# Optimization experiments

Measured on AMD Instinct MI355X. Metric: run time of the kernel, lower is better.

Reference implementation:

```python
import jax, jax.numpy as jnp
import numpy as np

N = 2048

def setup_inputs() -> dict:
    key = jax.random.key(0)
    k0, k1, k2, k3 = jax.random.split(key, 4)
    return {
        "input": jax.random.normal(k0, (N, N), dtype=jnp.float32),
        "weight1": jax.random.normal(k1, (N, N), dtype=jnp.float32),
        "weight2": jax.random.normal(k2, (N, N), dtype=jnp.float32),
        "weight3": jax.random.normal(k3, (N, N), dtype=jnp.float32),
    }

def reference(input, weight1, weight2, weight3):
    # Faithful translation of the torch DAG (duplicate mm kept: t4 == t2,
    # so t8 is mathematically zero, but we preserve the original math).
    t1 = input @ weight1
    t2 = input @ weight2
    t3 = weight3 @ weight3
    t4 = input @ weight2
    t5 = t1 * weight1
    t6 = (t5 @ input) * weight1
    t7 = t1 * t2 + t1 + t3
    t8 = t2 - t4
    t9 = t7 * t8 + t6 * t3
    t11 = t3 * t9
    t12 = t3 * (t1 @ input) * t6
    t13 = t7 + t11
    t14 = t8 + t12
    t15 = t13 + t14
    return t15
```

## Files before the change

### kernel.cpp

```cpp
#include <hip/hip_runtime.h>
#include <hip/hip_bf16.h>
#include <stdint.h>

#define NN 2048

typedef __bf16 bf16;
typedef __bf16 bf16x8 __attribute__((ext_vector_type(8)));
typedef __bf16 bf16x4 __attribute__((ext_vector_type(4)));
typedef float f32x4 __attribute__((ext_vector_type(4)));

__device__ __forceinline__ void async_copy16(bf16* lds, const bf16* g) {
    __builtin_amdgcn_global_load_lds(
        (const __attribute__((address_space(1))) unsigned int*)g,
        (__attribute__((address_space(3))) unsigned int*)lds,
        16, 0, 0);
}

__global__ void transpose_cast_kernel(const float* __restrict__ in,
                                      bf16* __restrict__ outT,
                                      bf16* __restrict__ outN) {
    __shared__ float tile[32][33];
    const int bx = blockIdx.x * 32, by = blockIdx.y * 32;
    const int tx = threadIdx.x, ty = threadIdx.y;
#pragma unroll
    for (int i = 0; i < 32; i += 8) {
        float v = in[(size_t)(by + ty + i) * NN + bx + tx];
        tile[ty + i][tx] = v;
        if (outN) outN[(size_t)(by + ty + i) * NN + bx + tx] = (bf16)v;
    }
    __syncthreads();
#pragma unroll
    for (int i = 0; i < 32; i += 8)
        outT[(size_t)(bx + ty + i) * NN + by + tx] = (bf16)tile[tx][ty + i];
}

struct GemmArgs {
    const bf16* A[3];
    const bf16* Bt[3];
    float*      C[3];
};

__global__ __launch_bounds__(256) void gemm_bt_batched(GemmArgs args) {
    const bf16* __restrict__ A  = args.A[blockIdx.z];
    const bf16* __restrict__ Bt = args.Bt[blockIdx.z];
    float* __restrict__ C       = args.C[blockIdx.z];

    __shared__ bf16 As[128 * 32];
    __shared__ bf16 Bs[128 * 32];

    const int t    = threadIdx.x;
    const int bm   = blockIdx.x * 128;
    const int bn   = blockIdx.y * 128;

    const int off0 = t * 8;
    const int row0 = off0 >> 5;
    const int col0 = off0 & 31;

    const bf16* gA0 = A  + (size_t)(bm + row0) * NN + col0;
    const bf16* gB0 = Bt + (size_t)(bn + row0) * NN + col0;

    const int wave = t >> 6;
    const int lane = t & 63;
    const int wm   = (wave >> 1) * 64;
    const int wn   = (wave & 1) * 64;
    const int lrow = lane & 15;
    const int q    = lane >> 4;

    f32x4 acc[4][4];
#pragma unroll
    for (int i = 0; i < 4; ++i)
#pragma unroll
        for (int j = 0; j < 4; ++j) acc[i][j] = (f32x4){0.f, 0.f, 0.f, 0.f};

    for (int k0 = 0; k0 < NN; k0 += 32) {
        async_copy16(&As[off0],            gA0 + k0);
        async_copy16(&As[off0 + 64 * 32],  gA0 + (size_t)64 * NN + k0);
        async_copy16(&Bs[off0],            gB0 + k0);
        async_copy16(&Bs[off0 + 64 * 32],  gB0 + (size_t)64 * NN + k0);
        __syncthreads();

        bf16x8 af[4], bfr[4];
#pragma unroll
        for (int i = 0; i < 4; ++i)
            af[i] = *(const bf16x8*)&As[(wm + i * 16 + lrow) * 32 + q * 8];
#pragma unroll
        for (int j = 0; j < 4; ++j)
            bfr[j] = *(const bf16x8*)&Bs[(wn + j * 16 + lrow) * 32 + q * 8];

#pragma unroll
        for (int i = 0; i < 4; ++i)
#pragma unroll
            for (int j = 0; j < 4; ++j)
                acc[i][j] = __builtin_amdgcn_mfma_f32_16x16x32_bf16(
                    af[i], bfr[j], acc[i][j], 0, 0, 0);
        __syncthreads();
    }

#pragma unroll
    for (int i = 0; i < 4; ++i)
#pragma unroll
        for (int j = 0; j < 4; ++j)
#pragma unroll
            for (int r = 0; r < 4; ++r)
                C[(size_t)(bm + wm + i * 16 + q * 4 + r) * NN +
                  (bn + wn + j * 16 + lrow)] = acc[i][j][r];
}

__global__ void post_m1_kernel(const float* __restrict__ M1,
                               const float* __restrict__ W1,
                               bf16* __restrict__ M1bf,
                               bf16* __restrict__ B1bf) {
    const size_t i = ((size_t)blockIdx.x * 256 + threadIdx.x) * 4;
    const float4 m = *(const float4*)&M1[i];
    const float4 w = *(const float4*)&W1[i];
    bf16x4 mb = {(bf16)m.x, (bf16)m.y, (bf16)m.z, (bf16)m.w};
    bf16x4 bb = {(bf16)(m.x * w.x), (bf16)(m.y * w.y),
                 (bf16)(m.z * w.z), (bf16)(m.w * w.w)};
    *(bf16x4*)&M1bf[i] = mb;
    *(bf16x4*)&B1bf[i] = bb;
}

__global__ void epilogue_kernel(const float* __restrict__ M1,
                                const float* __restrict__ M3,
                                const float* __restrict__ M4,
                                const float* __restrict__ M5,
                                const float* __restrict__ W1,
                                float* __restrict__ out) {
    const size_t i = ((size_t)blockIdx.x * 256 + threadIdx.x) * 4;
    const float4 m1 = *(const float4*)&M1[i];
    const float4 m3 = *(const float4*)&M3[i];
    const float4 m4 = *(const float4*)&M4[i];
    const float4 m5 = *(const float4*)&M5[i];
    const float4 w1 = *(const float4*)&W1[i];
    const float4 m2 = *(const float4*)&out[i];
    float4 r;
    r.x = m1.x * m2.x + m1.x + m3.x + m3.x * (m4.x * w1.x) * (m3.x + m5.x);
    r.y = m1.y * m2.y + m1.y + m3.y + m3.y * (m4.y * w1.y) * (m3.y + m5.y);
    r.z = m1.z * m2.z + m1.z + m3.z + m3.z * (m4.z * w1.z) * (m3.z + m5.z);
    r.w = m1.w * m2.w + m1.w + m3.w + m3.w * (m4.w * w1.w) * (m3.w + m5.w);
    *(float4*)&out[i] = r;
}

extern "C" void kernel_launch(void* const* d_in, const int* in_sizes, int n_in,
                              void* d_out, int out_size, void* d_ws, size_t ws_size,
                              hipStream_t stream) {
    const float* A  = (const float*)d_in[0];
    const float* W1 = (const float*)d_in[1];
    const float* W2 = (const float*)d_in[2];
    const float* W3 = (const float*)d_in[3];
    float* out = (float*)d_out;

    const size_t P = (size_t)NN * NN;
    char* ws = (char*)d_ws;

    bf16* Abf  = (bf16*)ws;
    bf16* At   = Abf + P;
    bf16* W1t  = At + P;
    bf16* W2t  = W1t + P;
    bf16* W3bf = W2t + P;
    bf16* W3t  = W3bf + P;
    float* M1  = (float*)(W3t + P);
    float* M3  = M1 + P;
    float* M4  = M3 + P;
    float* M5  = M4 + P;

    const dim3 tb(32, 8), tg(NN / 32, NN / 32);
    transpose_cast_kernel<<<tg, tb, 0, stream>>>(A,  At,  Abf);
    transpose_cast_kernel<<<tg, tb, 0, stream>>>(W1, W1t, nullptr);
    transpose_cast_kernel<<<tg, tb, 0, stream>>>(W2, W2t, nullptr);
    transpose_cast_kernel<<<tg, tb, 0, stream>>>(W3, W3t, W3bf);

    GemmArgs g3;
    g3.A[0] = Abf;  g3.Bt[0] = W1t; g3.C[0] = M1;
    g3.A[1] = Abf;  g3.Bt[1] = W2t; g3.C[1] = out;
    g3.A[2] = W3bf; g3.Bt[2] = W3t; g3.C[2] = M3;
    gemm_bt_batched<<<dim3(NN / 128, NN / 128, 3), 256, 0, stream>>>(g3);

    bf16* M1bf = W2t;
    bf16* B1bf = W3bf;
    post_m1_kernel<<<(P / 4) / 256, 256, 0, stream>>>(M1, W1, M1bf, B1bf);

    GemmArgs g2;
    g2.A[0] = M1bf; g2.Bt[0] = At; g2.C[0] = M5;
    g2.A[1] = B1bf; g2.Bt[1] = At; g2.C[1] = M4;
    g2.A[2] = M1bf; g2.Bt[2] = At; g2.C[2] = M5;
    gemm_bt_batched<<<dim3(NN / 128, NN / 128, 2), 256, 0, stream>>>(g2);

    epilogue_kernel<<<(P / 4) / 256, 256, 0, stream>>>(M1, M3, M4, M5, W1, out);
}
```

Measured before the change: 290.1 us.

## Use 128x64 GEMM tiles with XOR-swizzled LDS and batch transpose-cast launches

Shrinks the GEMM block tile from 128x128 to 128x64, which doubles the grid size so more CUs stay busy and each thread holds fewer accumulator registers. Adds an XOR swizzle on the LDS column index, applied to both the async global-to-LDS stores and the fragment reads, to reduce bank conflicts. Merges the four transpose-cast launches into one launch using a z-dimension. In exchange, A tiles are reloaded twice as often per output element, so per-FLOP global and LDS traffic goes up.

```diff
diff --git a/kernel.cpp b/kernel.cpp
--- a/kernel.cpp
+++ b/kernel.cpp
@@ -3,6 +3,9 @@
 #include <stdint.h>
 
 #define NN 2048
+#define BM 128
+#define BN 64
+#define BK 32
 
 typedef __bf16 bf16;
 typedef __bf16 bf16x8 __attribute__((ext_vector_type(8)));
@@ -16,9 +19,16 @@
         16, 0, 0);
 }
 
-__global__ void transpose_cast_kernel(const float* __restrict__ in,
-                                      bf16* __restrict__ outT,
-                                      bf16* __restrict__ outN) {
+struct CastArgs {
+    const float* in[4];
+    bf16*        outT[4];
+    bf16*        outN[4];
+};
+
+__global__ void transpose_cast_kernel(CastArgs args) {
+    const float* __restrict__ in = args.in[blockIdx.z];
+    bf16* __restrict__ outT      = args.outT[blockIdx.z];
+    bf16* __restrict__ outN      = args.outN[blockIdx.z];
     __shared__ float tile[32][33];
     const int bx = blockIdx.x * 32, by = blockIdx.y * 32;
     const int tx = threadIdx.x, ty = threadIdx.y;
@@ -45,16 +55,17 @@
     const bf16* __restrict__ Bt = args.Bt[blockIdx.z];
     float* __restrict__ C       = args.C[blockIdx.z];
 
-    __shared__ bf16 As[128 * 32];
-    __shared__ bf16 Bs[128 * 32];
-
-    const int t    = threadIdx.x;
-    const int bm   = blockIdx.x * 128;
-    const int bn   = blockIdx.y * 128;
-
+    __shared__ bf16 As[BM * BK];
+    __shared__ bf16 Bs[BN * BK];
+
+    const int t  = threadIdx.x;
+    const int bm = blockIdx.x * BM;
+    const int bn = blockIdx.y * BN;
+
+    const int row0 = t >> 2;
+    const int qp   = t & 3;
+    const int col0 = ((qp ^ ((row0 >> 1) & 3)) << 3);
     const int off0 = t * 8;
-    const int row0 = off0 >> 5;
-    const int col0 = off0 & 31;
 
     const bf16* gA0 = A  + (size_t)(bm + row0) * NN + col0;
     const bf16* gB0 = Bt + (size_t)(bn + row0) * NN + col0;
@@ -62,35 +73,35 @@
     const int wave = t >> 6;
     const int lane = t & 63;
     const int wm   = (wave >> 1) * 64;
-    const int wn   = (wave & 1) * 64;
+    const int wn   = (wave & 1) * 32;
     const int lrow = lane & 15;
     const int q    = lane >> 4;
-
-    f32x4 acc[4][4];
+    const int qe   = (q ^ ((lrow >> 1) & 3)) << 3;
+
+    f32x4 acc[4][2];
 #pragma unroll
     for (int i = 0; i < 4; ++i)
 #pragma unroll
-        for (int j = 0; j < 4; ++j) acc[i][j] = (f32x4){0.f, 0.f, 0.f, 0.f};
-
-    for (int k0 = 0; k0 < NN; k0 += 32) {
-        async_copy16(&As[off0],            gA0 + k0);
-        async_copy16(&As[off0 + 64 * 32],  gA0 + (size_t)64 * NN + k0);
-        async_copy16(&Bs[off0],            gB0 + k0);
-        async_copy16(&Bs[off0 + 64 * 32],  gB0 + (size_t)64 * NN + k0);
+        for (int j = 0; j < 2; ++j) acc[i][j] = (f32x4){0.f, 0.f, 0.f, 0.f};
+
+    for (int k0 = 0; k0 < NN; k0 += BK) {
+        async_copy16(&As[off0],           gA0 + k0);
+        async_copy16(&As[off0 + 64 * BK], gA0 + (size_t)64 * NN + k0);
+        async_copy16(&Bs[off0],           gB0 + k0);
         __syncthreads();
 
-        bf16x8 af[4], bfr[4];
+        bf16x8 af[4], bfr[2];
 #pragma unroll
         for (int i = 0; i < 4; ++i)
-            af[i] = *(const bf16x8*)&As[(wm + i * 16 + lrow) * 32 + q * 8];
-#pragma unroll
-        for (int j = 0; j < 4; ++j)
-            bfr[j] = *(const bf16x8*)&Bs[(wn + j * 16 + lrow) * 32 + q * 8];
+            af[i] = *(const bf16x8*)&As[(wm + i * 16 + lrow) * BK + qe];
+#pragma unroll
+        for (int j = 0; j < 2; ++j)
+            bfr[j] = *(const bf16x8*)&Bs[(wn + j * 16 + lrow) * BK + qe];
 
 #pragma unroll
         for (int i = 0; i < 4; ++i)
 #pragma unroll
-            for (int j = 0; j < 4; ++j)
+            for (int j = 0; j < 2; ++j)
                 acc[i][j] = __builtin_amdgcn_mfma_f32_16x16x32_bf16(
                     af[i], bfr[j], acc[i][j], 0, 0, 0);
         __syncthreads();
@@ -99,7 +110,7 @@
 #pragma unroll
     for (int i = 0; i < 4; ++i)
 #pragma unroll
-        for (int j = 0; j < 4; ++j)
+        for (int j = 0; j < 2; ++j)
 #pragma unroll
             for (int r = 0; r < 4; ++r)
                 C[(size_t)(bm + wm + i * 16 + q * 4 + r) * NN +
@@ -164,17 +175,18 @@
     float* M4  = M3 + P;
     float* M5  = M4 + P;
 
-    const dim3 tb(32, 8), tg(NN / 32, NN / 32);
-    transpose_cast_kernel<<<tg, tb, 0, stream>>>(A,  At,  Abf);
-    transpose_cast_kernel<<<tg, tb, 0, stream>>>(W1, W1t, nullptr);
-    transpose_cast_kernel<<<tg, tb, 0, stream>>>(W2, W2t, nullptr);
-    transpose_cast_kernel<<<tg, tb, 0, stream>>>(W3, W3t, W3bf);
+    CastArgs ca;
+    ca.in[0] = A;  ca.outT[0] = At;  ca.outN[0] = Abf;
+    ca.in[1] = W1; ca.outT[1] = W1t; ca.outN[1] = nullptr;
+    ca.in[2] = W2; ca.outT[2] = W2t; ca.outN[2] = nullptr;
+    ca.in[3] = W3; ca.outT[3] = W3t; ca.outN[3] = W3bf;
+    transpose_cast_kernel<<<dim3(NN / 32, NN / 32, 4), dim3(32, 8), 0, stream>>>(ca);
 
     GemmArgs g3;
     g3.A[0] = Abf;  g3.Bt[0] = W1t; g3.C[0] = M1;
     g3.A[1] = Abf;  g3.Bt[1] = W2t; g3.C[1] = out;
     g3.A[2] = W3bf; g3.Bt[2] = W3t; g3.C[2] = M3;
-    gemm_bt_batched<<<dim3(NN / 128, NN / 128, 3), 256, 0, stream>>>(g3);
+    gemm_bt_batched<<<dim3(NN / BM, NN / BN, 3), 256, 0, stream>>>(g3);
 
     bf16* M1bf = W2t;
     bf16* B1bf = W3bf;
@@ -184,7 +196,7 @@
     g2.A[0] = M1bf; g2.Bt[0] = At; g2.C[0] = M5;
     g2.A[1] = B1bf; g2.Bt[1] = At; g2.C[1] = M4;
     g2.A[2] = M1bf; g2.Bt[2] = At; g2.C[2] = M5;
-    gemm_bt_batched<<<dim3(NN / 128, NN / 128, 2), 256, 0, stream>>>(g2);
+    gemm_bt_batched<<<dim3(NN / BM, NN / BN, 2), 256, 0, stream>>>(g2);
 
     epilogue_kernel<<<(P / 4) / 256, 256, 0, stream>>>(M1, M3, M4, M5, W1, out);
 }
```

Result: faster. 273.4 us (-5.8%).
